# Performance work log

Measured on AMD Instinct MI355X. Metric: run time of the kernel, lower is better.

Reference implementation:

```python
import jax, jax.numpy as jnp
import numpy as np

HIDDEN = 1024
HEADS = 16
HEAD_DIM = HIDDEN // HEADS
SCALE = float(np.sqrt(HEAD_DIM))


def setup_inputs() -> dict:
    key = jax.random.key(0)
    ks = jax.random.split(key, 9)
    B, S = 2, 2048
    x = jax.random.normal(ks[0], (B, S, HIDDEN), dtype=jnp.float32)
    mask = jnp.ones((B, S, S), dtype=jnp.int32)
    init = 1.0 / np.sqrt(HIDDEN)
    def lin(k):
        kw, kb = jax.random.split(k)
        W = jax.random.uniform(kw, (HIDDEN, HIDDEN), jnp.float32, -init, init)
        b = jax.random.uniform(kb, (HIDDEN,), jnp.float32, -init, init)
        return W, b
    Wq, bq = lin(ks[1])
    Wk, bk = lin(ks[2])
    Wv, bv = lin(ks[3])
    Wo, bo = lin(ks[4])
    return {"x": x, "mask": mask, "Wq": Wq, "bq": bq, "Wk": Wk, "bk": bk,
            "Wv": Wv, "bv": bv, "Wo": Wo, "bo": bo}


def reference(x, mask, Wq, bq, Wk, bk, Wv, bv, Wo, bo):
    B, S, _ = x.shape
    # Linear projections, split into heads: [B, H, S, Dh]
    def proj(W, b):
        y = jnp.einsum('bsd,ed->bse', x, W) + b  # torch Linear: x @ W.T + b
        return y.reshape(B, S, HEADS, HEAD_DIM).transpose(0, 2, 1, 3)
    q = proj(Wq, bq)
    k = proj(Wk, bk)
    v = proj(Wv, bv)
    scores = jnp.einsum('bhqd,bhkd->bhqk', q, k) / SCALE  # [B,H,S,S]
    scores = jnp.where(mask[:, None, :, :] == 0, jnp.float32(-1e9), scores)
    attn = jax.nn.softmax(scores, axis=-1)
    # dropout is identity at inference (eval mode)
    out = jnp.einsum('bhqk,bhkd->bhqd', attn, v)
    out = out.transpose(0, 2, 1, 3).reshape(B, S, HIDDEN)
    return jnp.einsum('bsd,ed->bse', out, Wo) + bo
```

## Files before the change

kernel.cpp:

```cpp
#include <hip/hip_runtime.h>
#include <hip/hip_bf16.h>

typedef __attribute__((ext_vector_type(8))) short bf16x8;
typedef __attribute__((ext_vector_type(4))) float f32x4;
typedef __attribute__((ext_vector_type(16))) float f32x16;
typedef unsigned int uint;

typedef __attribute__((address_space(1))) void as1_void;
typedef __attribute__((address_space(3))) void as3_void;

__device__ __forceinline__ void gload16(const void* g, void* l) {
  __builtin_amdgcn_global_load_lds((as1_void*)(void*)g, (as3_void*)l, 16, 0, 0);
}

__device__ __forceinline__ f32x4 mfma16(bf16x8 a, bf16x8 b, f32x4 c) {
  return __builtin_amdgcn_mfma_f32_16x16x32_bf16(a, b, c, 0, 0, 0);
}

__device__ __forceinline__ f32x16 mfma32(bf16x8 a, bf16x8 b, f32x16 c) {
  return __builtin_amdgcn_mfma_f32_32x32x16_bf16(a, b, c, 0, 0, 0);
}

__global__ __launch_bounds__(256) void castf2b(const float* __restrict__ s,
                                               __hip_bfloat16* __restrict__ d, int n) {
  int i = (blockIdx.x * 256 + threadIdx.x) * 4;
  if (i >= n) return;
  float4 f = *reinterpret_cast<const float4*>(s + i);
  union { __hip_bfloat16 h[4]; uint2 u; } cv;
  cv.h[0] = __float2bfloat16(f.x);
  cv.h[1] = __float2bfloat16(f.y);
  cv.h[2] = __float2bfloat16(f.z);
  cv.h[3] = __float2bfloat16(f.w);
  *reinterpret_cast<uint2*>(d + i) = cv.u;
}

__global__ __launch_bounds__(256) void mask_pack(const int* __restrict__ m,
                                                 unsigned long long* __restrict__ bits) {
  int g = blockIdx.x * 256 + threadIdx.x;
  unsigned long long bal = __ballot(m[g] != 0);
  if ((threadIdx.x & 63) == 0) bits[g >> 6] = bal;
}

__global__ __launch_bounds__(256) void vtrans(const __hip_bfloat16* __restrict__ v,
                                              __hip_bfloat16* __restrict__ vt) {
  int bh = blockIdx.x >> 5;
  int s0 = (blockIdx.x & 31) * 64;
  __shared__ __align__(16) __hip_bfloat16 tile[64][72];
  const __hip_bfloat16* src = v + ((size_t)bh * 2048 + s0) * 64;
  int t = threadIdx.x;
#pragma unroll
  for (int i = 0; i < 2; i++) {
    int c = t + i * 256;
    int r = c >> 3, c8 = (c & 7) * 8;
    *reinterpret_cast<uint4*>(&tile[r][c8]) =
        *reinterpret_cast<const uint4*>(src + (size_t)r * 64 + c8);
  }
  __syncthreads();
  __hip_bfloat16* dst = vt + (size_t)bh * 64 * 2048 + s0;
#pragma unroll
  for (int i = 0; i < 2; i++) {
    int c = t + i * 256;
    int d = c >> 3, s8 = (c & 7) * 8;
    __hip_bfloat16 tmp[8] __attribute__((aligned(16)));
#pragma unroll
    for (int j = 0; j < 8; j++) tmp[j] = tile[s8 + j][d];
    *reinterpret_cast<uint4*>(dst + (size_t)d * 2048 + s8) =
        *reinterpret_cast<const uint4*>(tmp);
  }
}

template <int MODE>
__global__ __launch_bounds__(256) void gemm_bt(
    const __hip_bfloat16* __restrict__ A, const __hip_bfloat16* __restrict__ Bw,
    const float* __restrict__ bias0, const float* __restrict__ bias1,
    const float* __restrict__ bias2, __hip_bfloat16* __restrict__ out0,
    __hip_bfloat16* __restrict__ out1, __hip_bfloat16* __restrict__ out2,
    float* __restrict__ foutp, int M, int N, int K) {
  __shared__ __align__(16) __hip_bfloat16 Alds[128 * 64];
  __shared__ __align__(16) __hip_bfloat16 Blds[128 * 64];
  const int t = threadIdx.x;
  const int lane = t & 63;
  const int w = t >> 6;
  const int wr = w >> 1, wc = w & 1;
  const int l15 = lane & 15, lhi = lane >> 4;
  const int Nt = N >> 7;
  const int bm = (int)blockIdx.x / Nt, bn = (int)blockIdx.x % Nt;
  const int m0 = bm * 128, n0 = bn * 128;

  const f32x4 fzero = {0.f, 0.f, 0.f, 0.f};
  f32x4 acc[4][4];
#pragma unroll
  for (int mi = 0; mi < 4; mi++)
#pragma unroll
    for (int ni = 0; ni < 4; ni++) acc[mi][ni] = fzero;

  for (int k0 = 0; k0 < K; k0 += 64) {
#pragma unroll
    for (int i = 0; i < 4; i++) {
      int c = t + i * 256;
      int r = c >> 3, c8 = (c & 7) * 8;
      gload16(A + (size_t)(m0 + r) * K + k0 + c8, (char*)Alds + c * 16);
      gload16(Bw + (size_t)(n0 + r) * K + k0 + c8, (char*)Blds + c * 16);
    }
    __syncthreads();
#pragma unroll
    for (int kk = 0; kk < 2; kk++) {
      bf16x8 af[4], bfr[4];
#pragma unroll
      for (int mi = 0; mi < 4; mi++)
        af[mi] = *reinterpret_cast<const bf16x8*>(
            &Alds[(wr * 64 + mi * 16 + l15) * 64 + kk * 32 + lhi * 8]);
#pragma unroll
      for (int ni = 0; ni < 4; ni++)
        bfr[ni] = *reinterpret_cast<const bf16x8*>(
            &Blds[(wc * 64 + ni * 16 + l15) * 64 + kk * 32 + lhi * 8]);
#pragma unroll
      for (int mi = 0; mi < 4; mi++)
#pragma unroll
        for (int ni = 0; ni < 4; ni++)
          acc[mi][ni] = mfma16(af[mi], bfr[ni], acc[mi][ni]);
    }
    __syncthreads();
  }

#pragma unroll
  for (int mi = 0; mi < 4; mi++) {
#pragma unroll
    for (int ni = 0; ni < 4; ni++) {
#pragma unroll
      for (int r = 0; r < 4; r++) {
        int gr = m0 + wr * 64 + mi * 16 + lhi * 4 + r;
        int gc = n0 + wc * 64 + ni * 16 + l15;
        float v = acc[mi][ni][r];
        if (MODE == 0) {
          int seg = gc >> 10, e = gc & 1023, h = e >> 6, d = e & 63;
          int b = gr >> 11, s = gr & 2047;
          size_t idx = (((size_t)(b * 16 + h)) * 2048 + s) * 64 + d;
          if (seg == 0)
            out0[idx] = __float2bfloat16((v + bias0[e]) * 0.125f);
          else if (seg == 1)
            out1[idx] = __float2bfloat16(v + bias1[e]);
          else
            out2[idx] = __float2bfloat16(v + bias2[e]);
        } else {
          foutp[(size_t)gr * N + gc] = v + bias0[gc];
        }
      }
    }
  }
}

__global__ __launch_bounds__(256) void attn2(
    const __hip_bfloat16* __restrict__ Q, const __hip_bfloat16* __restrict__ Kk,
    const __hip_bfloat16* __restrict__ VT,
    const unsigned long long* __restrict__ mb, __hip_bfloat16* __restrict__ ctx) {
  int bx = blockIdx.x;
  int bid = (bx & 7) * 64 + (bx >> 3);
  int bh = bid >> 4, qc = bid & 15;
  int b = bh >> 4, h = bh & 15;
  int lane = threadIdx.x & 63, w = threadIdx.x >> 6;
  int l31 = lane & 31, lh = lane >> 5, lh4 = lh * 4;
  int q0 = qc * 128 + w * 32;

  const __hip_bfloat16* Qrow = Q + ((size_t)bh * 2048 + q0 + l31) * 64 + lh * 8;
  const __hip_bfloat16* Krow = Kk + ((size_t)bh * 2048 + l31) * 64 + lh * 8;
  const __hip_bfloat16* V0 = VT + ((size_t)bh * 64 + l31) * 2048 + lh * 8;
  const __hip_bfloat16* V1 = V0 + 32 * 2048;
  const unsigned long long* Mrow = mb + ((size_t)b * 2048 + q0 + l31) * 32;

  bf16x8 qf[4];
#pragma unroll
  for (int ck = 0; ck < 4; ck++)
    qf[ck] = *reinterpret_cast<const bf16x8*>(Qrow + ck * 16);

  f32x16 o0 = {}, o1 = {};
  float mrun = -3.0e38f, lrun = 0.f;

  unsigned long long mw = Mrow[0], mwn = 0;
  bool skipm = __all(mw == ~0ull);

  auto comp = [&](const bf16x8* kf, const bf16x8* vf, int half) {
    f32x16 s = {};
#pragma unroll
    for (int ck = 0; ck < 4; ck++) s = mfma32(kf[ck], qf[ck], s);
    if (!skipm) {
      uint mh = (uint)(mw >> half) >> lh4;
#pragma unroll
      for (int r = 0; r < 16; r++) {
        int cr = (r & 3) + 8 * (r >> 2);
        if (!((mh >> cr) & 1u)) s[r] = -1e9f;
      }
    }
    float pmax = s[0];
#pragma unroll
    for (int r = 1; r < 16; r++) pmax = fmaxf(pmax, s[r]);
    pmax = fmaxf(pmax, __shfl_xor(pmax, 32));
    if (!__all(pmax <= mrun + 8.0f)) {
      float nm = fmaxf(mrun, pmax);
      float scl = __expf(mrun - nm);
      mrun = nm;
      lrun *= scl;
#pragma unroll
      for (int r = 0; r < 16; r++) {
        int cr = (r & 3) + 8 * (r >> 2);
        float sr = __shfl(scl, cr + lh4);
        o0[r] *= sr;
        o1[r] *= sr;
      }
    }
    float p[16];
    float ts = 0.f;
#pragma unroll
    for (int r = 0; r < 16; r++) {
      p[r] = __expf(s[r] - mrun);
      ts += p[r];
    }
    ts += __shfl_xor(ts, 32);
    lrun += ts;
    uint x0, x1, x2, x3, y0, y1, y2, y3;
    asm("v_cvt_pk_bf16_f32 %0, %1, %2" : "=v"(x0) : "v"(p[0]), "v"(p[1]));
    asm("v_cvt_pk_bf16_f32 %0, %1, %2" : "=v"(y0) : "v"(p[4]), "v"(p[5]));
    asm("v_cvt_pk_bf16_f32 %0, %1, %2" : "=v"(x1) : "v"(p[2]), "v"(p[3]));
    asm("v_cvt_pk_bf16_f32 %0, %1, %2" : "=v"(y1) : "v"(p[6]), "v"(p[7]));
    asm("v_cvt_pk_bf16_f32 %0, %1, %2" : "=v"(x2) : "v"(p[8]), "v"(p[9]));
    asm("v_cvt_pk_bf16_f32 %0, %1, %2" : "=v"(y2) : "v"(p[12]), "v"(p[13]));
    asm("v_cvt_pk_bf16_f32 %0, %1, %2" : "=v"(x3) : "v"(p[10]), "v"(p[11]));
    asm("v_cvt_pk_bf16_f32 %0, %1, %2" : "=v"(y3) : "v"(p[14]), "v"(p[15]));
    asm volatile("v_permlane32_swap_b32 %0, %1" : "+v"(x0), "+v"(y0));
    asm volatile("v_permlane32_swap_b32 %0, %1" : "+v"(x1), "+v"(y1));
    asm volatile("v_permlane32_swap_b32 %0, %1" : "+v"(x2), "+v"(y2));
    asm volatile("v_permlane32_swap_b32 %0, %1" : "+v"(x3), "+v"(y3));
    union { uint u[4]; bf16x8 v8; } pa0, pa1;
    pa0.u[0] = x0; pa0.u[1] = x1; pa0.u[2] = y0; pa0.u[3] = y1;
    pa1.u[0] = x2; pa1.u[1] = x3; pa1.u[2] = y2; pa1.u[3] = y3;
    o0 = mfma32(pa0.v8, vf[0], o0);
    o0 = mfma32(pa1.v8, vf[1], o0);
    o1 = mfma32(pa0.v8, vf[2], o1);
    o1 = mfma32(pa1.v8, vf[3], o1);
  };

  bf16x8 kfA[4], vfA[4], kfB[4], vfB[4];
#pragma unroll
  for (int ck = 0; ck < 4; ck++)
    kfA[ck] = *reinterpret_cast<const bf16x8*>(Krow + ck * 16);
  vfA[0] = *reinterpret_cast<const bf16x8*>(V0);
  vfA[1] = *reinterpret_cast<const bf16x8*>(V0 + 16);
  vfA[2] = *reinterpret_cast<const bf16x8*>(V1);
  vfA[3] = *reinterpret_cast<const bf16x8*>(V1 + 16);

  for (int i = 0; i < 32; ++i) {
    const int t1 = 2 * i + 1;
#pragma unroll
    for (int ck = 0; ck < 4; ck++)
      kfB[ck] = *reinterpret_cast<const bf16x8*>(Krow + t1 * 2048 + ck * 16);
    vfB[0] = *reinterpret_cast<const bf16x8*>(V0 + t1 * 32);
    vfB[1] = *reinterpret_cast<const bf16x8*>(V0 + t1 * 32 + 16);
    vfB[2] = *reinterpret_cast<const bf16x8*>(V1 + t1 * 32);
    vfB[3] = *reinterpret_cast<const bf16x8*>(V1 + t1 * 32 + 16);
    mwn = Mrow[i + 1 < 32 ? i + 1 : 31];

    comp(kfA, vfA, 0);

    if (i < 31) {
      const int t2 = 2 * i + 2;
#pragma unroll
      for (int ck = 0; ck < 4; ck++)
        kfA[ck] = *reinterpret_cast<const bf16x8*>(Krow + t2 * 2048 + ck * 16);
      vfA[0] = *reinterpret_cast<const bf16x8*>(V0 + t2 * 32);
      vfA[1] = *reinterpret_cast<const bf16x8*>(V0 + t2 * 32 + 16);
      vfA[2] = *reinterpret_cast<const bf16x8*>(V1 + t2 * 32);
      vfA[3] = *reinterpret_cast<const bf16x8*>(V1 + t2 * 32 + 16);
    }

    comp(kfB, vfB, 32);

    mw = mwn;
    skipm = __all(mw == ~0ull);
  }

  float linv = 1.0f / lrun;
  size_t obase = ((size_t)b * 2048 + q0) * 1024 + (size_t)h * 64 + l31;
#pragma unroll
  for (int r = 0; r < 16; r++) {
    int cr = (r & 3) + 8 * (r >> 2);
    int rho = cr + lh4;
    float li = __shfl(linv, rho);
    ctx[obase + (size_t)rho * 1024] = __float2bfloat16(o0[r] * li);
    ctx[obase + (size_t)rho * 1024 + 32] = __float2bfloat16(o1[r] * li);
  }
}

extern "C" void kernel_launch(void* const* d_in, const int* in_sizes, int n_in,
                              void* d_out, int out_size, void* d_ws,
                              size_t ws_size, hipStream_t stream) {
  const float* x = (const float*)d_in[0];
  const int* mask = (const int*)d_in[1];
  const float* Wq = (const float*)d_in[2];
  const float* bq = (const float*)d_in[3];
  const float* Wk = (const float*)d_in[4];
  const float* bk = (const float*)d_in[5];
  const float* Wv = (const float*)d_in[6];
  const float* bv = (const float*)d_in[7];
  const float* Wo = (const float*)d_in[8];
  const float* bo = (const float*)d_in[9];
  float* out = (float*)d_out;
  char* ws = (char*)d_ws;

  __hip_bfloat16* xb   = (__hip_bfloat16*)(ws);
  __hip_bfloat16* wqkv = (__hip_bfloat16*)(ws + 8388608);
  __hip_bfloat16* wo   = (__hip_bfloat16*)(ws + 14680064);
  __hip_bfloat16* qws  = (__hip_bfloat16*)(ws + 16777216);
  __hip_bfloat16* kws  = (__hip_bfloat16*)(ws + 25165824);
  __hip_bfloat16* vtmp = (__hip_bfloat16*)(ws + 33554432);
  __hip_bfloat16* vt   = (__hip_bfloat16*)(ws + 41943040);
  __hip_bfloat16* ctx  = (__hip_bfloat16*)(ws + 50331648);
  unsigned long long* mbits = (unsigned long long*)(ws + 58720256);

  castf2b<<<4096, 256, 0, stream>>>(x, xb, 4194304);
  castf2b<<<1024, 256, 0, stream>>>(Wq, wqkv, 1048576);
  castf2b<<<1024, 256, 0, stream>>>(Wk, wqkv + 1048576, 1048576);
  castf2b<<<1024, 256, 0, stream>>>(Wv, wqkv + 2097152, 1048576);
  castf2b<<<1024, 256, 0, stream>>>(Wo, wo, 1048576);
  mask_pack<<<32768, 256, 0, stream>>>(mask, mbits);

  gemm_bt<0><<<768, 256, 0, stream>>>(xb, wqkv, bq, bk, bv, qws, kws, vtmp,
                                      nullptr, 4096, 3072, 1024);
  vtrans<<<1024, 256, 0, stream>>>(vtmp, vt);
  attn2<<<512, 256, 0, stream>>>(qws, kws, vt, mbits, ctx);
  gemm_bt<1><<<256, 256, 0, stream>>>(ctx, wo, bo, nullptr, nullptr, nullptr,
                                      nullptr, nullptr, out, 4096, 1024, 1024);
}
```

Before: 352.2 us.

## Split attention KV range across warps and merge partial softmax in LDS

The attention kernel now assigns each block 64 query rows instead of 128. Two warp pairs each process half of the key/value sequence and combine their partial outputs through shared memory using the running max and sum. This doubles the grid to 1024 blocks, aimed at better CU occupancy on the large GPU, at the cost of extra LDS traffic, two barriers and a rescale step. Separately, the four weight-cast launches are merged into one kernel to cut launch overhead.

```diff
diff --git a/kernel.cpp b/kernel.cpp
--- a/kernel.cpp
+++ b/kernel.cpp
@@ -25,6 +25,23 @@
                                                __hip_bfloat16* __restrict__ d, int n) {
   int i = (blockIdx.x * 256 + threadIdx.x) * 4;
   if (i >= n) return;
+  float4 f = *reinterpret_cast<const float4*>(s + i);
+  union { __hip_bfloat16 h[4]; uint2 u; } cv;
+  cv.h[0] = __float2bfloat16(f.x);
+  cv.h[1] = __float2bfloat16(f.y);
+  cv.h[2] = __float2bfloat16(f.z);
+  cv.h[3] = __float2bfloat16(f.w);
+  *reinterpret_cast<uint2*>(d + i) = cv.u;
+}
+
+__global__ __launch_bounds__(256) void castw(
+    const float* __restrict__ Wq, const float* __restrict__ Wk,
+    const float* __restrict__ Wv, const float* __restrict__ Wo,
+    __hip_bfloat16* __restrict__ wqkv, __hip_bfloat16* __restrict__ wo) {
+  int seg = blockIdx.x >> 10;
+  int i = ((blockIdx.x & 1023) * 256 + threadIdx.x) * 4;
+  const float* s = seg == 0 ? Wq : seg == 1 ? Wk : seg == 2 ? Wv : Wo;
+  __hip_bfloat16* d = seg < 3 ? wqkv + seg * 1048576 : wo;
   float4 f = *reinterpret_cast<const float4*>(s + i);
   union { __hip_bfloat16 h[4]; uint2 u; } cv;
   cv.h[0] = __float2bfloat16(f.x);
@@ -155,18 +172,28 @@
     const __hip_bfloat16* __restrict__ VT,
     const unsigned long long* __restrict__ mb, __hip_bfloat16* __restrict__ ctx) {
   int bx = blockIdx.x;
-  int bid = (bx & 7) * 64 + (bx >> 3);
-  int bh = bid >> 4, qc = bid & 15;
+  int bid = (bx & 7) * 128 + (bx >> 3);
+  int bh = bid >> 5, qc = bid & 31;
   int b = bh >> 4, h = bh & 15;
   int lane = threadIdx.x & 63, w = threadIdx.x >> 6;
   int l31 = lane & 31, lh = lane >> 5, lh4 = lh * 4;
-  int q0 = qc * 128 + w * 32;
+  int wsb = w & 1;
+  int kvh = w >> 1;
+  int q0 = qc * 64 + wsb * 32;
+  int kvbase = kvh * 1024;
+
+  __shared__ float olds[2][32][64];
+  __shared__ float mlds[2][2][32];
+  __shared__ float llds[2][2][32];
 
   const __hip_bfloat16* Qrow = Q + ((size_t)bh * 2048 + q0 + l31) * 64 + lh * 8;
-  const __hip_bfloat16* Krow = Kk + ((size_t)bh * 2048 + l31) * 64 + lh * 8;
-  const __hip_bfloat16* V0 = VT + ((size_t)bh * 64 + l31) * 2048 + lh * 8;
+  const __hip_bfloat16* Krow =
+      Kk + ((size_t)bh * 2048 + kvbase + l31) * 64 + lh * 8;
+  const __hip_bfloat16* V0 =
+      VT + ((size_t)bh * 64 + l31) * 2048 + kvbase + lh * 8;
   const __hip_bfloat16* V1 = V0 + 32 * 2048;
-  const unsigned long long* Mrow = mb + ((size_t)b * 2048 + q0 + l31) * 32;
+  const unsigned long long* Mrow =
+      mb + ((size_t)b * 2048 + q0 + l31) * 32 + kvh * 16;
 
   bf16x8 qf[4];
 #pragma unroll
@@ -179,12 +206,12 @@
   unsigned long long mw = Mrow[0], mwn = 0;
   bool skipm = __all(mw == ~0ull);
 
-  auto comp = [&](const bf16x8* kf, const bf16x8* vf, int half) {
+  auto comp = [&](const bf16x8* kf, const bf16x8* vf, int sh) {
     f32x16 s = {};
 #pragma unroll
     for (int ck = 0; ck < 4; ck++) s = mfma32(kf[ck], qf[ck], s);
     if (!skipm) {
-      uint mh = (uint)(mw >> half) >> lh4;
+      uint mh = (uint)(mw >> sh) >> lh4;
 #pragma unroll
       for (int r = 0; r < 16; r++) {
         int cr = (r & 3) + 8 * (r >> 2);
@@ -248,7 +275,7 @@
   vfA[2] = *reinterpret_cast<const bf16x8*>(V1);
   vfA[3] = *reinterpret_cast<const bf16x8*>(V1 + 16);
 
-  for (int i = 0; i < 32; ++i) {
+  for (int i = 0; i < 16; ++i) {
     const int t1 = 2 * i + 1;
 #pragma unroll
     for (int ck = 0; ck < 4; ck++)
@@ -257,11 +284,11 @@
     vfB[1] = *reinterpret_cast<const bf16x8*>(V0 + t1 * 32 + 16);
     vfB[2] = *reinterpret_cast<const bf16x8*>(V1 + t1 * 32);
     vfB[3] = *reinterpret_cast<const bf16x8*>(V1 + t1 * 32 + 16);
-    mwn = Mrow[i + 1 < 32 ? i + 1 : 31];
+    mwn = Mrow[i + 1 < 16 ? i + 1 : 15];
 
     comp(kfA, vfA, 0);
 
-    if (i < 31) {
+    if (i < 15) {
       const int t2 = 2 * i + 2;
 #pragma unroll
       for (int ck = 0; ck < 4; ck++)
@@ -278,15 +305,39 @@
     skipm = __all(mw == ~0ull);
   }
 
-  float linv = 1.0f / lrun;
-  size_t obase = ((size_t)b * 2048 + q0) * 1024 + (size_t)h * 64 + l31;
-#pragma unroll
-  for (int r = 0; r < 16; r++) {
-    int cr = (r & 3) + 8 * (r >> 2);
-    int rho = cr + lh4;
-    float li = __shfl(linv, rho);
-    ctx[obase + (size_t)rho * 1024] = __float2bfloat16(o0[r] * li);
-    ctx[obase + (size_t)rho * 1024 + 32] = __float2bfloat16(o1[r] * li);
+  if (lh == 0) {
+    mlds[wsb][kvh][l31] = mrun;
+    llds[wsb][kvh][l31] = lrun;
+  }
+  __syncthreads();
+  float mA = mlds[wsb][0][l31], mB = mlds[wsb][1][l31];
+  float lA = llds[wsb][0][l31], lB = llds[wsb][1][l31];
+  float mN = fmaxf(mA, mB);
+  float aA = __expf(mA - mN), aB = __expf(mB - mN);
+  if (kvh) {
+#pragma unroll
+    for (int r = 0; r < 16; r++) {
+      int cr = (r & 3) + 8 * (r >> 2);
+      float ar = __shfl(aB, cr + lh4);
+      olds[wsb][r][lane] = o0[r] * ar;
+      olds[wsb][16 + r][lane] = o1[r] * ar;
+    }
+  }
+  __syncthreads();
+  if (!kvh) {
+    float linv = 1.0f / (lA * aA + lB * aB);
+    size_t obase = ((size_t)b * 2048 + q0) * 1024 + (size_t)h * 64 + l31;
+#pragma unroll
+    for (int r = 0; r < 16; r++) {
+      int cr = (r & 3) + 8 * (r >> 2);
+      int rho = cr + lh4;
+      float ar = __shfl(aA, rho);
+      float li = __shfl(linv, rho);
+      float v0 = o0[r] * ar + olds[wsb][r][lane];
+      float v1 = o1[r] * ar + olds[wsb][16 + r][lane];
+      ctx[obase + (size_t)rho * 1024] = __float2bfloat16(v0 * li);
+      ctx[obase + (size_t)rho * 1024 + 32] = __float2bfloat16(v1 * li);
+    }
   }
 }
 
@@ -317,16 +368,13 @@
   unsigned long long* mbits = (unsigned long long*)(ws + 58720256);
 
   castf2b<<<4096, 256, 0, stream>>>(x, xb, 4194304);
-  castf2b<<<1024, 256, 0, stream>>>(Wq, wqkv, 1048576);
-  castf2b<<<1024, 256, 0, stream>>>(Wk, wqkv + 1048576, 1048576);
-  castf2b<<<1024, 256, 0, stream>>>(Wv, wqkv + 2097152, 1048576);
-  castf2b<<<1024, 256, 0, stream>>>(Wo, wo, 1048576);
+  castw<<<4096, 256, 0, stream>>>(Wq, Wk, Wv, Wo, wqkv, wo);
   mask_pack<<<32768, 256, 0, stream>>>(mask, mbits);
 
   gemm_bt<0><<<768, 256, 0, stream>>>(xb, wqkv, bq, bk, bv, qws, kws, vtmp,
                                       nullptr, 4096, 3072, 1024);
   vtrans<<<1024, 256, 0, stream>>>(vtmp, vt);
-  attn2<<<512, 256, 0, stream>>>(qws, kws, vt, mbits, ctx);
+  attn2<<<1024, 256, 0, stream>>>(qws, kws, vt, mbits, ctx);
   gemm_bt<1><<<256, 256, 0, stream>>>(ctx, wo, bo, nullptr, nullptr, nullptr,
                                       nullptr, nullptr, out, 4096, 1024, 1024);
 }
```

After: 346.1 us. Within noise of the previous version (-1.7%).
